# Kernel tuning notes

Hardware: AMD Instinct MI355X
Metric: run time of the kernel (lower is better)

## Reference

```python
import jax, jax.numpy as jnp
import numpy as np

Q_N, S_N, U_N = 5000, 1000, 2000          # questions, skills, users
NQ = NS = NU = NQ2 = 8                     # neighbor fan-outs
D = 100                                    # emb_dim
AGG_HOPS = 3
RANK_K = 10
S_PER_Q = 4                                # skills per question in qs_table
B, T = 32, 100
NEG = -1e30


def linear(x, W, b):
    return x @ W + b


def _forward(fl, it):
    (uq_table, emb_q, emb_q2, emb_s, emb_u, emb_r,
     w1_q, w2_q, w_c, w_p, w_n,
     lstm_Wih, lstm_Whh, lstm_bih, lstm_bhh,
     fusion_W, fusion_b, agg_W, agg_b, agg_last_W, agg_last_b,
     query_W, query_b, key_W, key_b, attn_W, attn_b) = fl
    (user, question, response, mask,
     q_neighbors, s_neighbors, u_neighbors, q_neighbors_2, skill_idx_table) = it

    K_all = emb_q[question]  # [B,T,D] question embeddings for recap scoring

    def build_nodes(root, tabA, tabB):
        # multi-hop neighbor id gather: [B], [B,n0], [B,n0,n1], [B,n0,n1,n2]
        nodes = [root]
        for i in range(AGG_HOPS):
            tab = tabA if i % 2 == 0 else tabB
            nodes.append(tab[nodes[-1]])
        return nodes

    def aggregate(nodes, embA, embB, weighted):
        embs = [(embA if i % 2 == 0 else embB)[n] for i, n in enumerate(nodes)]
        for i in range(AGG_HOPS):
            for j in range(AGG_HOPS - i):
                nb = embs[j + 1]
                if weighted:  # uq branch: edge weights from dense uq_table
                    self_ids, nb_ids = nodes[j], nodes[j + 1]
                    exp_self = jnp.broadcast_to(self_ids[..., None], nb_ids.shape)
                    uid = exp_self if j % 2 == 0 else nb_ids
                    qid = nb_ids if j % 2 == 0 else exp_self
                    w = uq_table[uid, qid]  # [..., 3]
                    fw = w_c * w[..., 0:1] + w_p * w[..., 1:2] + w_n * w[..., 2:3]
                    nb = nb * fw
                s = nb.mean(axis=-2) + embs[j]
                embs[j] = jax.nn.relu(linear(s, agg_W[j], agg_b[j]))
        return jax.nn.relu(linear(embs[0], agg_last_W, agg_last_b))

    def predict(qs_concat, hist, hist_valid):
        # GIKT-style bi-attention readout (source truncated; see notes)
        k = linear(qs_concat, key_W, key_b)    # [B,Nq,D]
        q = linear(hist, query_W, query_b)     # [B,Nh,D]
        Nq, Nh = k.shape[1], q.shape[1]
        feat = jnp.concatenate([
            jnp.broadcast_to(k[:, :, None, :], (B, Nq, Nh, D)),
            jnp.broadcast_to(q[:, None, :, :], (B, Nq, Nh, D))], axis=-1)
        logits = (feat @ attn_W + attn_b)[..., 0]          # [B,Nq,Nh]
        logits = jnp.where(hist_valid[:, None, :], logits, NEG)
        alpha = jax.nn.softmax(logits.reshape(B, -1), axis=1).reshape(B, Nq, Nh)
        inner = jnp.einsum('bqd,bhd->bqh', qs_concat, hist)
        return jax.nn.sigmoid(jnp.sum(alpha * inner, axis=(1, 2)))

    def step(carry, t):
        h, c, state_hist = carry
        m = mask[:, t][:, None]
        u_t, q_t, r_t = user[:, t], question[:, t], response[:, t]
        emb_qt = jnp.where(m, aggregate(build_nodes(q_t, q_neighbors, s_neighbors), emb_q, emb_s, False), emb_q[q_t])
        emb_qt2 = jnp.where(m, aggregate(build_nodes(u_t, u_neighbors, q_neighbors_2), emb_u, emb_q2, True), emb_q2[q_t])
        emb_hat = w1_q * emb_qt + w2_q * emb_qt2
        e_t = jax.nn.relu(linear(jnp.concatenate([emb_hat, emb_r[r_t]], axis=1), fusion_W, fusion_b))
        # LSTMCell (torch gate order i,f,g,o); dropout is identity in eval
        gates = e_t @ lstm_Wih + lstm_bih + h @ lstm_Whh + lstm_bhh
        ig, fg, gg, og = jnp.split(gates, 4, axis=1)
        c_n = jax.nn.sigmoid(fg) * c + jax.nn.sigmoid(ig) * jnp.tanh(gg)
        h_n = jax.nn.sigmoid(og) * jnp.tanh(c_n)
        h = jnp.where(m, h_n, h)
        c = jnp.where(m, c_n, c)
        state_hist = jax.lax.dynamic_update_slice_in_dim(state_hist, h[:, None, :], t, axis=1)
        # recap: question + related skills, current state + top-k history
        q_next = question[:, t + 1]
        emb_qnext = emb_q[q_next]
        qs_concat = jnp.concatenate([emb_qnext[:, None, :], emb_s[skill_idx_table[q_next]]], axis=1)  # [B,1+S_PER_Q,D]
        scores = jnp.einsum('btd,bd->bt', K_all, emb_qnext)
        scores = jnp.where(jnp.arange(T)[None, :] < t, scores, NEG)  # only past steps
        top_s, idx = jax.lax.top_k(scores, RANK_K)
        sel = jnp.take_along_axis(state_hist, idx[:, :, None], axis=1)  # [B,K,D]
        hist = jnp.concatenate([h[:, None, :], sel], axis=1)             # [B,K+1,D]
        hist_valid = jnp.concatenate([jnp.ones((B, 1), bool), top_s > NEG / 2], axis=1)
        return (h, c, state_hist), predict(qs_concat, hist, hist_valid)

    init = (jnp.zeros((B, D), jnp.float32), jnp.zeros((B, D), jnp.float32),
            jnp.zeros((B, T, D), jnp.float32))
    _, ys = jax.lax.scan(jax.checkpoint(step), init, jnp.arange(T - 1))
    return jnp.zeros((B, T), jnp.float32).at[:, 1:].set(ys.T)


def _p(k, shape, scale=0.1):
    return scale * jax.random.normal(k, shape, dtype=jnp.float32)


def setup_inputs():
    key = jax.random.key(0)
    ks = jax.random.split(key, 24)
    rng = np.random.default_rng(0)
    # qs_table with exactly S_PER_Q distinct skills per question -> static skill index table
    qs_idx = np.argsort(rng.random((Q_N, S_N)), axis=1)[:, :S_PER_Q]
    return dict(
        user=jax.random.randint(ks[0], (B, T), 0, U_N),
        question=jax.random.randint(ks[1], (B, T), 0, Q_N),
        response=jax.random.randint(ks[2], (B, T), 0, 2),
        mask=jnp.ones((B, T), dtype=bool),
        q_neighbors=jax.random.randint(ks[3], (Q_N, NQ), 0, S_N),
        s_neighbors=jax.random.randint(ks[4], (S_N, NS), 0, Q_N),
        u_neighbors=jax.random.randint(ks[5], (U_N, NU), 0, Q_N),
        q_neighbors_2=jax.random.randint(ks[6], (Q_N, NQ2), 0, U_N),
        skill_idx_table=jnp.asarray(qs_idx, dtype=jnp.int32),
        uq_table=jax.random.uniform(ks[7], (U_N, Q_N, 3), dtype=jnp.float32),
        emb_q=_p(ks[8], (Q_N, D)), emb_q2=_p(ks[9], (Q_N, D)),
        emb_s=_p(ks[10], (S_N, D)), emb_u=_p(ks[11], (U_N, D)), emb_r=_p(ks[12], (2, D)),
        w1_q=jnp.asarray(0.5, jnp.float32), w2_q=jnp.asarray(0.5, jnp.float32),
        w_c=jnp.asarray(0.33, jnp.float32), w_p=jnp.asarray(0.33, jnp.float32), w_n=jnp.asarray(0.33, jnp.float32),
        lstm_Wih=_p(ks[13], (D, 4 * D)), lstm_Whh=_p(ks[14], (D, 4 * D)),
        lstm_bih=jnp.zeros(4 * D, jnp.float32), lstm_bhh=jnp.zeros(4 * D, jnp.float32),
        fusion_W=_p(ks[15], (2 * D, D)), fusion_b=jnp.zeros(D, jnp.float32),
        agg_W=_p(ks[16], (AGG_HOPS, D, D)), agg_b=jnp.zeros((AGG_HOPS, D), jnp.float32),
        agg_last_W=_p(ks[17], (D, D)), agg_last_b=jnp.zeros(D, jnp.float32),
        query_W=_p(ks[18], (D, D)), query_b=jnp.zeros(D, jnp.float32),
        key_W=_p(ks[19], (D, D)), key_b=jnp.zeros(D, jnp.float32),
        attn_W=_p(ks[20], (2 * D, 1)), attn_b=jnp.zeros(1, jnp.float32),
    )


def reference(user, question, response, mask, q_neighbors, s_neighbors, u_neighbors,
              q_neighbors_2, skill_idx_table, uq_table, emb_q, emb_q2, emb_s, emb_u, emb_r,
              w1_q, w2_q, w_c, w_p, w_n, lstm_Wih, lstm_Whh, lstm_bih, lstm_bhh,
              fusion_W, fusion_b, agg_W, agg_b, agg_last_W, agg_last_b,
              query_W, query_b, key_W, key_b, attn_W, attn_b):
    fl = (uq_table, emb_q, emb_q2, emb_s, emb_u, emb_r,
          w1_q, w2_q, w_c, w_p, w_n,
          lstm_Wih, lstm_Whh, lstm_bih, lstm_bhh,
          fusion_W, fusion_b, agg_W, agg_b, agg_last_W, agg_last_b,
          query_W, query_b, key_W, key_b, attn_W, attn_b)
    it = (user, question, response, mask,
          q_neighbors, s_neighbors, u_neighbors, q_neighbors_2, skill_idx_table)
    return _forward(fl, it)
```

## Files before the change

### kernel.cpp

```cpp
#include <hip/hip_runtime.h>
#include <math.h>

#define Q_N 5000
#define S_N 1000
#define U_N 2000
#define D   100
#define B   32
#define T   100
#define NBT (B*(T-1))
#define NEG_F (-1e30f)

#define NB_Z2Q ((Q_N+15)/16)
#define NB_Z2U ((U_N+15)/16)
#define NB_Y1Q ((S_N+15)/16)
#define NB_Y1U ((Q_N+15)/16)

#define GPROJ_SZ (NBT*4*D)
#define H_SZ     (B*T*D)
#define QAGG_SZ  (Q_N*D)
#define UAGG_SZ  (U_N*D)
#define Z2Q_SZ   (Q_N*D)
#define Z2U_SZ   (U_N*D)
#define Y1Q_SZ   (S_N*D)
#define Y1U_SZ   (Q_N*D)
#define WHT_SZ   (4*D*D)

__device__ __forceinline__ void fma4(float4& a, float s, const float4 w) {
    a.x = fmaf(s, w.x, a.x); a.y = fmaf(s, w.y, a.y);
    a.z = fmaf(s, w.z, a.z); a.w = fmaf(s, w.w, a.w);
}
__device__ __forceinline__ float4 relu4(float4 v) {
    v.x = v.x > 0.f ? v.x : 0.f; v.y = v.y > 0.f ? v.y : 0.f;
    v.z = v.z > 0.f ? v.z : 0.f; v.w = v.w > 0.f ? v.w : 0.f;
    return v;
}
__device__ __forceinline__ float4 add4(float4 a, float4 b) {
    a.x += b.x; a.y += b.y; a.z += b.z; a.w += b.w; return a;
}

template<int K>
__device__ __forceinline__ void mv100_b256(const float* __restrict__ W,
                                           const float* __restrict__ bias,
                                           const float* __restrict__ src,
                                           float* __restrict__ dst,
                                           float* __restrict__ part)
{
    const int tid = threadIdx.x;
    const int c4  = tid & 31;
    const int ks  = tid >> 5;
    const int col0 = (4*c4 < 96) ? 4*c4 : 96;
    float4 acc = {0.f,0.f,0.f,0.f};
#pragma unroll 2
    for (int d = ks*4; d < K; d += 32) {
        const float4 sv = *(const float4*)&src[d];
        const float4 w0 = *(const float4*)&W[(d+0)*D + col0];
        const float4 w1 = *(const float4*)&W[(d+1)*D + col0];
        const float4 w2 = *(const float4*)&W[(d+2)*D + col0];
        const float4 w3 = *(const float4*)&W[(d+3)*D + col0];
        fma4(acc, sv.x, w0); fma4(acc, sv.y, w1);
        fma4(acc, sv.z, w2); fma4(acc, sv.w, w3);
    }
    *(float4*)&part[ks*D + col0] = acc;
    __syncthreads();
    if (tid < D) {
        float v = bias[tid];
#pragma unroll
        for (int k = 0; k < 8; ++k) v += part[k*D + tid];
        dst[tid] = v > 0.f ? v : 0.f;
    }
    __syncthreads();
}

struct __align__(16) Stage16 {
    float x[16*D];
    int   nb[128];
    float fw[128];
};

template<int UQ_MODE>
__device__ __forceinline__ void stage16(Stage16& sh, int row0, int N,
        const float* __restrict__ selfEmb, const float* __restrict__ nbEmb,
        const int* __restrict__ tab,
        const float* __restrict__ uq, float wc, float wp, float wn,
        const float* __restrict__ W, const float* __restrict__ bias,
        float* __restrict__ out)
{
    const int tid = threadIdx.x;
    if (tid < 128) {
        const int i = tid >> 3, k = tid & 7;
        int v = row0 + i; if (v >= N) v = N - 1;
        const int nbv = tab[v*8 + k];
        sh.nb[tid] = nbv;
        float f = 0.125f;
        if (UQ_MODE == 1) {
            const float* w = &uq[(v*Q_N + nbv)*3];
            f = 0.125f*(wc*w[0] + wp*w[1] + wn*w[2]);
        } else if (UQ_MODE == 2) {
            const float* w = &uq[(nbv*Q_N + v)*3];
            f = 0.125f*(wc*w[0] + wp*w[1] + wn*w[2]);
        }
        sh.fw[tid] = f;
    }
    __syncthreads();
    const int c4   = tid & 31;
    const int rowg = tid >> 5;
    const int col0 = (4*c4 < 96) ? 4*c4 : 96;
#pragma unroll
    for (int rr = 0; rr < 2; ++rr) {
        const int i = rowg + 8*rr;
        int v = row0 + i; if (v >= N) v = N - 1;
        float4 acc = *(const float4*)&selfEmb[v*D + col0];
#pragma unroll
        for (int k = 0; k < 8; ++k)
            fma4(acc, sh.fw[i*8 + k], *(const float4*)&nbEmb[sh.nb[i*8 + k]*D + col0]);
        *(float4*)&sh.x[i*D + col0] = acc;
    }
    __syncthreads();
    float4 a0 = {0.f,0.f,0.f,0.f}, a1 = {0.f,0.f,0.f,0.f};
#pragma unroll 1
    for (int d = 0; d < D; d += 4) {
        const float4 w0 = *(const float4*)&W[(d+0)*D + col0];
        const float4 w1 = *(const float4*)&W[(d+1)*D + col0];
        const float4 w2 = *(const float4*)&W[(d+2)*D + col0];
        const float4 w3 = *(const float4*)&W[(d+3)*D + col0];
        const float4 s0 = *(const float4*)&sh.x[rowg*D + d];
        const float4 s1 = *(const float4*)&sh.x[(rowg+8)*D + d];
        fma4(a0, s0.x, w0); fma4(a0, s0.y, w1); fma4(a0, s0.z, w2); fma4(a0, s0.w, w3);
        fma4(a1, s1.x, w0); fma4(a1, s1.y, w1); fma4(a1, s1.z, w2); fma4(a1, s1.w, w3);
    }
    const float4 bb = *(const float4*)&bias[col0];
    {
        int v = row0 + rowg; if (v >= N) v = N - 1;
        *(float4*)&out[v*D + col0] = relu4(add4(a0, bb));
        v = row0 + rowg + 8; if (v >= N) v = N - 1;
        *(float4*)&out[v*D + col0] = relu4(add4(a1, bb));
    }
}

__global__ __launch_bounds__(256, 6)
void kStageA(const int* __restrict__ qnb, const int* __restrict__ snb,
             const int* __restrict__ unb, const int* __restrict__ qnb2,
             const float* __restrict__ emb_q, const float* __restrict__ emb_q2,
             const float* __restrict__ emb_s, const float* __restrict__ emb_u,
             const float* __restrict__ uq,
             const float* __restrict__ wcp, const float* __restrict__ wpp,
             const float* __restrict__ wnp,
             const float* __restrict__ aggW, const float* __restrict__ aggB,
             float* __restrict__ z2q, float* __restrict__ z2u,
             float* __restrict__ y1q0, float* __restrict__ y1u0)
{
    __shared__ Stage16 sh;
    const float wc = wcp[0], wp = wpp[0], wn = wnp[0];
    int b = blockIdx.x;
    if (b < NB_Z2Q) {
        stage16<0>(sh, b*16, Q_N, emb_q, emb_s, qnb, uq, wc, wp, wn,
                   aggW + 2*D*D, aggB + 2*D, z2q);
        return;
    }
    b -= NB_Z2Q;
    if (b < NB_Z2U) {
        stage16<1>(sh, b*16, U_N, emb_u, emb_q2, unb, uq, wc, wp, wn,
                   aggW + 2*D*D, aggB + 2*D, z2u);
        return;
    }
    b -= NB_Z2U;
    if (b < NB_Y1Q) {
        stage16<0>(sh, b*16, S_N, emb_s, emb_q, snb, uq, wc, wp, wn,
                   aggW + 1*D*D, aggB + 1*D, y1q0);
        return;
    }
    b -= NB_Y1Q;
    stage16<2>(sh, b*16, Q_N, emb_q2, emb_u, qnb2, uq, wc, wp, wn,
               aggW + 1*D*D, aggB + 1*D, y1u0);
}

__global__ __launch_bounds__(256, 6)
void kStageB(const int* __restrict__ snb, const int* __restrict__ qnb2,
             const float* __restrict__ uq,
             const float* __restrict__ wcp, const float* __restrict__ wpp,
             const float* __restrict__ wnp,
             const float* __restrict__ aggW, const float* __restrict__ aggB,
             const float* __restrict__ z2q, const float* __restrict__ z2u,
             const float* __restrict__ y1q0, const float* __restrict__ y1u0,
             float* __restrict__ y1q1, float* __restrict__ y1u1)
{
    __shared__ Stage16 sh;
    const float wc = wcp[0], wp = wpp[0], wn = wnp[0];
    int b = blockIdx.x;
    if (b < NB_Y1Q) {
        stage16<0>(sh, b*16, S_N, y1q0, z2q, snb, uq, wc, wp, wn,
                   aggW + 1*D*D, aggB + 1*D, y1q1);
        return;
    }
    b -= NB_Y1Q;
    stage16<2>(sh, b*16, Q_N, y1u0, z2u, qnb2, uq, wc, wp, wn,
               aggW + 1*D*D, aggB + 1*D, y1u1);
}

__global__ void kMarkInit(int* __restrict__ marks)
{
    const int i = blockIdx.x*256 + threadIdx.x;
    if (i < Q_N + U_N) marks[i] = 0;
}
__global__ void kMark(const int* __restrict__ question, const int* __restrict__ user,
                      int* __restrict__ qmark, int* __restrict__ umark)
{
    const int bt = blockIdx.x*256 + threadIdx.x;
    if (bt < NBT) {
        const int b = bt / (T-1), t = bt % (T-1);
        qmark[question[b*T + t]] = 1;
        umark[user[b*T + t]] = 1;
    }
}

__global__ __launch_bounds__(256)
void kTransW(const float* __restrict__ Whh, float* __restrict__ WhhT)
{
    const int i = blockIdx.x*256 + threadIdx.x;
    if (i < 4*D*D) {
        const int c = i / D, d = i - c*D;
        WhhT[i] = Whh[d*4*D + c];
    }
}

struct __align__(16) RootSh {
    float e0[D];
    float part[8*D];
    int   nb[8];
    float fw[8];
};

template<bool WEIGHTED>
__device__ __forceinline__ void rootchain(RootSh& sh, int root,
        const int* __restrict__ tab,
        const float* __restrict__ selfEmb, const float* __restrict__ lvl1Emb,
        const float* __restrict__ y0, const float* __restrict__ y1,
        const float* __restrict__ W0, const float* __restrict__ b0,
        const float* __restrict__ WL, const float* __restrict__ bL,
        const float* __restrict__ uq, float wc, float wp, float wn,
        float* __restrict__ outrow)
{
    const int tid = threadIdx.x;
    if (tid < 8) {
        const int a = tab[root*8 + tid];
        sh.nb[tid] = a;
        float f = 0.125f;
        if (WEIGHTED) {
            const float* w = &uq[(root*Q_N + a)*3];
            f = 0.125f*(wc*w[0] + wp*w[1] + wn*w[2]);
        }
        sh.fw[tid] = f;
    }
    __syncthreads();
    const int c4 = tid & 31;
    const int col0 = (4*c4 < 96) ? 4*c4 : 96;
    if (tid < 32) {
        float4 acc = *(const float4*)&selfEmb[root*D + col0];
#pragma unroll
        for (int k = 0; k < 8; ++k)
            fma4(acc, sh.fw[k], *(const float4*)&lvl1Emb[sh.nb[k]*D + col0]);
        *(float4*)&sh.e0[col0] = acc;
    }
    __syncthreads();
    mv100_b256<D>(W0, b0, sh.e0, sh.e0, sh.part);
    if (tid < 32) {
        float4 acc = *(const float4*)&sh.e0[col0];
#pragma unroll
        for (int k = 0; k < 8; ++k)
            fma4(acc, sh.fw[k], *(const float4*)&y0[sh.nb[k]*D + col0]);
        *(float4*)&sh.e0[col0] = acc;
    }
    __syncthreads();
    mv100_b256<D>(W0, b0, sh.e0, sh.e0, sh.part);
    if (tid < 32) {
        float4 acc = *(const float4*)&sh.e0[col0];
#pragma unroll
        for (int k = 0; k < 8; ++k)
            fma4(acc, sh.fw[k], *(const float4*)&y1[sh.nb[k]*D + col0]);
        *(float4*)&sh.e0[col0] = acc;
    }
    __syncthreads();
    mv100_b256<D>(W0, b0, sh.e0, sh.e0, sh.part);
    mv100_b256<D>(WL, bL, sh.e0, outrow, sh.part);
}

__global__ __launch_bounds__(256, 6)
void kRoot(const int* __restrict__ qmark, const int* __restrict__ umark,
           const int* __restrict__ qnb, const int* __restrict__ unb,
           const float* __restrict__ emb_q, const float* __restrict__ emb_u,
           const float* __restrict__ emb_s, const float* __restrict__ emb_q2,
           const float* __restrict__ y1q0, const float* __restrict__ y1q1,
           const float* __restrict__ y1u0, const float* __restrict__ y1u1,
           const float* __restrict__ uq,
           const float* __restrict__ wcp, const float* __restrict__ wpp,
           const float* __restrict__ wnp,
           const float* __restrict__ aggW, const float* __restrict__ aggB,
           const float* __restrict__ aggLW, const float* __restrict__ aggLb,
           float* __restrict__ qagg, float* __restrict__ uagg)
{
    __shared__ RootSh sh;
    const int b = blockIdx.x;
    if (b < Q_N) {
        if (!qmark[b]) return;
        rootchain<false>(sh, b, qnb, emb_q, emb_s, y1q0, y1q1,
                         aggW, aggB, aggLW, aggLb,
                         uq, 0.f, 0.f, 0.f, qagg + b*D);
    } else {
        const int u = b - Q_N;
        if (!umark[u]) return;
        rootchain<true>(sh, u, unb, emb_u, emb_q2, y1u0, y1u1,
                        aggW, aggB, aggLW, aggLb,
                        uq, wcp[0], wpp[0], wnp[0], uagg + u*D);
    }
}

__global__ __launch_bounds__(256)
void kFuse(const int* __restrict__ question, const int* __restrict__ user,
           const int* __restrict__ response,
           const float* __restrict__ qagg, const float* __restrict__ uagg,
           const float* __restrict__ emb_r,
           const float* __restrict__ w1p, const float* __restrict__ w2p,
           const float* __restrict__ fusW, const float* __restrict__ fusb,
           const float* __restrict__ Wih, const float* __restrict__ bih,
           float* __restrict__ gproj)
{
    __shared__ __align__(16) float xcat[2*D];
    __shared__ __align__(16) float evec[D];
    __shared__ __align__(16) float part[8*D];
    const int bt = blockIdx.x;
    const int b = bt / (T-1);
    const int t = bt % (T-1);
    const int tid = threadIdx.x;
    const int q = question[b*T + t];
    const int u = user[b*T + t];
    const int r = response[b*T + t];
    const float w1 = w1p[0], w2 = w2p[0];
    const int c4 = tid & 31;
    const int col0 = (4*c4 < 96) ? 4*c4 : 96;
    if (tid < 32) {
        float4 qa = *(const float4*)&qagg[q*D + col0];
        float4 ua = *(const float4*)&uagg[u*D + col0];
        float4 x; x.x = w1*qa.x + w2*ua.x; x.y = w1*qa.y + w2*ua.y;
        x.z = w1*qa.z + w2*ua.z; x.w = w1*qa.w + w2*ua.w;
        *(float4*)&xcat[col0] = x;
    } else if (tid < 64) {
        *(float4*)&xcat[D + col0] = *(const float4*)&emb_r[r*D + col0];
    }
    __syncthreads();
    mv100_b256<2*D>(fusW, fusb, xcat, evec, part);

    const int ks = tid >> 7, cw = tid & 127;
    if (cw < D) {
        float4 acc = {0.f,0.f,0.f,0.f};
#pragma unroll 5
        for (int dd = 0; dd < D/2; ++dd) {
            const int d = ks*(D/2) + dd;
            fma4(acc, evec[d], *(const float4*)&Wih[d*4*D + 4*cw]);
        }
        *(float4*)&part[ks*4*D + 4*cw] = acc;
    }
    __syncthreads();
    for (int i = tid; i < 4*D; i += 256) {
        gproj[bt*4*D + i] = part[i] + part[4*D + i] + bih[i];
    }
}

__global__ __launch_bounds__(256)
void kFold(const float* __restrict__ keyW, const float* __restrict__ queryW,
           const float* __restrict__ attnW, float* __restrict__ vk, float* __restrict__ vq)
{
    const int tid = threadIdx.x;
    if (tid < D) {
        float a = 0.f;
        for (int e = 0; e < D; ++e) a = fmaf(keyW[tid*D + e], attnW[e], a);
        vk[tid] = a;
    } else if (tid < 2*D) {
        const int d = tid - D;
        float a = 0.f;
        for (int e = 0; e < D; ++e) a = fmaf(queryW[d*D + e], attnW[D + e], a);
        vq[d] = a;
    }
}

#define KB_LDW(m) const float4 w##m = wvp[m];
#define KB_FMA(m) { const float4 hv = hvp[m]; \
    a0 = fmaf(hv.x, w##m.x, a0); a1 = fmaf(hv.y, w##m.y, a1); \
    a2 = fmaf(hv.z, w##m.z, a2); a3 = fmaf(hv.w, w##m.w, a3); }

__global__ __launch_bounds__(512, 1)
void kB(const float* __restrict__ gproj, const float* __restrict__ WhhT,
        const float* __restrict__ bhh, float* __restrict__ H)
{
    __shared__ __align__(16) float hbuf[D];
    __shared__ float gates[4*D];
    const int b = blockIdx.x;
    const int tid = threadIdx.x;
    const bool on = tid < 4*D;
    const int col = on ? tid : (4*D - 1);
    const float4* wvp = (const float4*)&WhhT[col*D];
    KB_LDW(0)  KB_LDW(1)  KB_LDW(2)  KB_LDW(3)  KB_LDW(4)
    KB_LDW(5)  KB_LDW(6)  KB_LDW(7)  KB_LDW(8)  KB_LDW(9)
    KB_LDW(10) KB_LDW(11) KB_LDW(12) KB_LDW(13) KB_LDW(14)
    KB_LDW(15) KB_LDW(16) KB_LDW(17) KB_LDW(18) KB_LDW(19)
    KB_LDW(20) KB_LDW(21) KB_LDW(22) KB_LDW(23) KB_LDW(24)
    const float bb = bhh[col];
    float creg = 0.f;
    if (tid < D) hbuf[tid] = 0.f;
    float g = on ? gproj[(b*(T-1) + 0)*4*D + col] : 0.f;
    __syncthreads();
#pragma unroll 1
    for (int t = 0; t < T-1; ++t) {
        {
            float a0 = g + bb, a1 = 0.f, a2 = 0.f, a3 = 0.f;
            const float4* hvp = (const float4*)hbuf;
            KB_FMA(0)  KB_FMA(1)  KB_FMA(2)  KB_FMA(3)  KB_FMA(4)
            KB_FMA(5)  KB_FMA(6)  KB_FMA(7)  KB_FMA(8)  KB_FMA(9)
            KB_FMA(10) KB_FMA(11) KB_FMA(12) KB_FMA(13) KB_FMA(14)
            KB_FMA(15) KB_FMA(16) KB_FMA(17) KB_FMA(18) KB_FMA(19)
            KB_FMA(20) KB_FMA(21) KB_FMA(22) KB_FMA(23) KB_FMA(24)
            if (on) gates[tid] = (a0 + a1) + (a2 + a3);
        }
        __syncthreads();
        if (t + 1 < T-1 && on) g = gproj[(b*(T-1) + t + 1)*4*D + col];
        if (tid < D) {
            const float ig = 1.f/(1.f + expf(-gates[tid]));
            const float fg = 1.f/(1.f + expf(-gates[D   + tid]));
            const float gg = tanhf(gates[2*D + tid]);
            const float og = 1.f/(1.f + expf(-gates[3*D + tid]));
            const float cn = fg*creg + ig*gg;
            const float hn = og*tanhf(cn);
            creg = cn;
            hbuf[tid] = hn;
            H[(b*T + t)*D + tid] = hn;
        }
        __syncthreads();
    }
}

__global__ __launch_bounds__(128)
void kC(const int* __restrict__ question, const int* __restrict__ skill_tab,
        const float* __restrict__ emb_q, const float* __restrict__ emb_s,
        const float* __restrict__ H, const float* __restrict__ vk,
        const float* __restrict__ vq, float* __restrict__ out)
{
    __shared__ __align__(16) float qs[5*D];
    __shared__ __align__(16) float hist[11*D];
    __shared__ float scores[T];
    __shared__ float kdot[5], qdot[11];
    __shared__ int   topi[10];
    __shared__ float topv[10];
    const int blk = blockIdx.x;
    const int b = blk / (T-1);
    const int t = blk % (T-1);
    const int tid = threadIdx.x;
    const int qn = question[b*T + t + 1];

    for (int i = tid; i < 5*D; i += 128) {
        const int rr = i / D, d = i % D;
        if (rr == 0) qs[i] = emb_q[qn*D + d];
        else         qs[i] = emb_s[skill_tab[qn*4 + (rr-1)]*D + d];
    }
    __syncthreads();

    for (int tau = tid; tau < T; tau += 128) {
        float sc = NEG_F;
        if (tau < t) {
            const float4* rowp = (const float4*)&emb_q[question[b*T + tau]*D];
            float acc = 0.f;
#pragma unroll 1
            for (int d4 = 0; d4 < D/4; ++d4) {
                const float4 a  = rowp[d4];
                const float4 qv = *(const float4*)&qs[d4*4];
                acc += a.x*qv.x + a.y*qv.y + a.z*qv.z + a.w*qv.w;
            }
            sc = acc;
        }
        scores[tau] = sc;
    }
    __syncthreads();

    for (int k = 0; k < 10; ++k) {
        if (tid < 64) {
            float v = scores[tid]; int idx = tid;
            if (tid + 64 < T) {
                const float v2 = scores[tid + 64];
                if (v2 > v) { v = v2; idx = tid + 64; }
            }
            for (int off = 32; off > 0; off >>= 1) {
                const float ov = __shfl_xor(v, off);
                const int   oi = __shfl_xor(idx, off);
                if (ov > v || (ov == v && oi < idx)) { v = ov; idx = oi; }
            }
            if (tid == 0) { topi[k] = idx; topv[k] = v; scores[idx] = NEG_F; }
        }
        __syncthreads();
    }

    for (int i = tid; i < 11*D; i += 128) {
        const int j = i / D, d = i % D;
        float v;
        if (j == 0) v = H[(b*T + t)*D + d];
        else        v = (topv[j-1] > -5e29f) ? H[(b*T + topi[j-1])*D + d] : 0.f;
        hist[i] = v;
    }
    __syncthreads();

    {
        const int dj = tid >> 3, ks = tid & 7;
        const float* vec = (dj < 5) ? &qs[dj*D] : &hist[(dj-5)*D];
        const float* vv  = (dj < 5) ? vk : vq;
        float a = 0.f;
#pragma unroll
        for (int d = ks; d < D; d += 8) a = fmaf(vec[d], vv[d], a);
        a += __shfl_xor(a, 1); a += __shfl_xor(a, 2); a += __shfl_xor(a, 4);
        if (ks == 0) { if (dj < 5) kdot[dj] = a; else qdot[dj-5] = a; }
    }
    __syncthreads();

    if (tid < 64) {
        const int i = tid / 11, j = tid - i*11;
        const bool act = tid < 55;
        const bool valid = act && (j == 0 || topv[j-1] > -5e29f);
        float logit = valid ? (kdot[i] + qdot[j]) : NEG_F;
        float mx = logit;
        for (int off = 32; off > 0; off >>= 1) mx = fmaxf(mx, __shfl_xor(mx, off));
        const float e = valid ? expf(logit - mx) : 0.f;
        float inner = 0.f;
        if (act) {
#pragma unroll
            for (int d4 = 0; d4 < D/4; ++d4) {
                const float4 a4 = *(const float4*)&qs[i*D + d4*4];
                const float4 h4 = *(const float4*)&hist[j*D + d4*4];
                inner += a4.x*h4.x + a4.y*h4.y + a4.z*h4.z + a4.w*h4.w;
            }
        }
        float num = e * inner;
        float den = e;
        for (int off = 32; off > 0; off >>= 1) {
            num += __shfl_xor(num, off);
            den += __shfl_xor(den, off);
        }
        if (tid == 0) {
            out[b*T + t + 1] = 1.f/(1.f + expf(-(num/den)));
            if (t == 0) out[b*T] = 0.f;
        }
    }
}

extern "C" void kernel_launch(void* const* d_in, const int* in_sizes, int n_in,
                              void* d_out, int out_size, void* d_ws, size_t ws_size,
                              hipStream_t stream)
{
    const int*   user     = (const int*)d_in[0];
    const int*   question = (const int*)d_in[1];
    const int*   response = (const int*)d_in[2];
    const int*   qnb   = (const int*)d_in[4];
    const int*   snb   = (const int*)d_in[5];
    const int*   unb   = (const int*)d_in[6];
    const int*   qnb2  = (const int*)d_in[7];
    const int*   skill = (const int*)d_in[8];
    const float* uq    = (const float*)d_in[9];
    const float* emb_q  = (const float*)d_in[10];
    const float* emb_q2 = (const float*)d_in[11];
    const float* emb_s  = (const float*)d_in[12];
    const float* emb_u  = (const float*)d_in[13];
    const float* emb_r  = (const float*)d_in[14];
    const float* w1 = (const float*)d_in[15];
    const float* w2 = (const float*)d_in[16];
    const float* wc = (const float*)d_in[17];
    const float* wp = (const float*)d_in[18];
    const float* wn = (const float*)d_in[19];
    const float* Wih = (const float*)d_in[20];
    const float* Whh = (const float*)d_in[21];
    const float* bih = (const float*)d_in[22];
    const float* bhh = (const float*)d_in[23];
    const float* fusW = (const float*)d_in[24];
    const float* fusb = (const float*)d_in[25];
    const float* aggW = (const float*)d_in[26];
    const float* aggB = (const float*)d_in[27];
    const float* aggLW = (const float*)d_in[28];
    const float* aggLb = (const float*)d_in[29];
    const float* queryW = (const float*)d_in[30];
    const float* keyW   = (const float*)d_in[32];
    const float* attnW  = (const float*)d_in[34];

    float* ws    = (float*)d_ws;
    float* gproj = ws;
    float* H     = gproj + GPROJ_SZ;
    float* vk    = H + H_SZ;
    float* vq    = vk + D;
    float* qagg  = vq + D;
    float* uagg  = qagg + QAGG_SZ;
    float* z2q   = uagg + UAGG_SZ;
    float* z2u   = z2q + Z2Q_SZ;
    float* y1q0  = z2u + Z2U_SZ;
    float* y1q1  = y1q0 + Y1Q_SZ;
    float* y1u0  = y1q1 + Y1Q_SZ;
    float* y1u1  = y1u0 + Y1U_SZ;
    float* whhT  = y1u1 + Y1U_SZ;
    int*   qmark = (int*)(whhT + WHT_SZ);
    int*   umark = qmark + Q_N;
    float* out   = (float*)d_out;

    const size_t need = (size_t)(GPROJ_SZ + H_SZ + 2*D + QAGG_SZ + UAGG_SZ
                       + Z2Q_SZ + Z2U_SZ + 2*Y1Q_SZ + 2*Y1U_SZ + WHT_SZ)*sizeof(float)
                       + (size_t)(Q_N + U_N)*sizeof(int);
    if (ws_size < need) return;

    kMarkInit<<<dim3((Q_N + U_N + 255)/256), dim3(256), 0, stream>>>(qmark);
    kMark<<<dim3((NBT + 255)/256), dim3(256), 0, stream>>>(question, user, qmark, umark);
    kTransW<<<dim3((4*D*D + 255)/256), dim3(256), 0, stream>>>(Whh, whhT);
    kStageA<<<dim3(NB_Z2Q + NB_Z2U + NB_Y1Q + NB_Y1U), dim3(256), 0, stream>>>(
        qnb, snb, unb, qnb2, emb_q, emb_q2, emb_s, emb_u, uq, wc, wp, wn,
        aggW, aggB, z2q, z2u, y1q0, y1u0);
    kStageB<<<dim3(NB_Y1Q + NB_Y1U), dim3(256), 0, stream>>>(
        snb, qnb2, uq, wc, wp, wn, aggW, aggB, z2q, z2u, y1q0, y1u0, y1q1, y1u1);
    kRoot<<<dim3(Q_N + U_N), dim3(256), 0, stream>>>(
        qmark, umark, qnb, unb, emb_q, emb_u, emb_s, emb_q2,
        y1q0, y1q1, y1u0, y1u1, uq, wc, wp, wn,
        aggW, aggB, aggLW, aggLb, qagg, uagg);
    kFold<<<dim3(1), dim3(256), 0, stream>>>(keyW, queryW, attnW, vk, vq);
    kFuse<<<dim3(NBT), dim3(256), 0, stream>>>(question, user, response, qagg, uagg,
        emb_r, w1, w2, fusW, fusb, Wih, bih, gproj);
    kB<<<dim3(B), dim3(512), 0, stream>>>(gproj, whhT, bhh, H);
    kC<<<dim3(NBT), dim3(128), 0, stream>>>(question, skill, emb_q, emb_s, H, vk, vq, out);
}
```

Baseline: 279.9 us.

## Fuse setup kernels and broadcast LSTM hidden state via readlane in recurrence

Merges the mark, weight-transpose and attention-fold kernels into one setup launch, cutting launch count. In the serial LSTM kernel, each wave loads the hidden vector once from shared memory as float2 per lane and broadcasts elements with readlane instead of issuing many LDS float4 reads per thread. Gate activations are moved into the 400-thread matvec phase so the 100-thread update phase only does the cell math. The readlane path adds scalar-register traffic and changes the occupancy attributes.

```diff
diff --git a/kernel.cpp b/kernel.cpp
--- a/kernel.cpp
+++ b/kernel.cpp
@@ -14,6 +14,8 @@
 #define NB_Z2U ((U_N+15)/16)
 #define NB_Y1Q ((S_N+15)/16)
 #define NB_Y1U ((Q_N+15)/16)
+#define NB_MK ((NBT+255)/256)
+#define NB_TW ((4*D*D+255)/256)
 
 #define GPROJ_SZ (NBT*4*D)
 #define H_SZ     (B*T*D)
@@ -202,24 +204,44 @@
     const int i = blockIdx.x*256 + threadIdx.x;
     if (i < Q_N + U_N) marks[i] = 0;
 }
-__global__ void kMark(const int* __restrict__ question, const int* __restrict__ user,
-                      int* __restrict__ qmark, int* __restrict__ umark)
-{
-    const int bt = blockIdx.x*256 + threadIdx.x;
-    if (bt < NBT) {
-        const int b = bt / (T-1), t = bt % (T-1);
-        qmark[question[b*T + t]] = 1;
-        umark[user[b*T + t]] = 1;
-    }
-}
 
 __global__ __launch_bounds__(256)
-void kTransW(const float* __restrict__ Whh, float* __restrict__ WhhT)
-{
-    const int i = blockIdx.x*256 + threadIdx.x;
-    if (i < 4*D*D) {
-        const int c = i / D, d = i - c*D;
-        WhhT[i] = Whh[d*4*D + c];
+void kSetup(const int* __restrict__ question, const int* __restrict__ user,
+            int* __restrict__ qmark, int* __restrict__ umark,
+            const float* __restrict__ Whh, float* __restrict__ WhhT,
+            const float* __restrict__ keyW, const float* __restrict__ queryW,
+            const float* __restrict__ attnW,
+            float* __restrict__ vk, float* __restrict__ vq)
+{
+    int bkt = blockIdx.x;
+    const int tid = threadIdx.x;
+    if (bkt < NB_MK) {
+        const int bt = bkt*256 + tid;
+        if (bt < NBT) {
+            const int b = bt / (T-1), t = bt % (T-1);
+            qmark[question[b*T + t]] = 1;
+            umark[user[b*T + t]] = 1;
+        }
+        return;
+    }
+    bkt -= NB_MK;
+    if (bkt < NB_TW) {
+        const int i = bkt*256 + tid;
+        if (i < 4*D*D) {
+            const int c = i / D, d = i - c*D;
+            WhhT[i] = Whh[d*4*D + c];
+        }
+        return;
+    }
+    if (tid < D) {
+        float a = 0.f;
+        for (int e = 0; e < D; ++e) a = fmaf(keyW[tid*D + e], attnW[e], a);
+        vk[tid] = a;
+    } else if (tid < 2*D) {
+        const int d = tid - D;
+        float a = 0.f;
+        for (int e = 0; e < D; ++e) a = fmaf(queryW[d*D + e], attnW[D + e], a);
+        vq[d] = a;
     }
 }
 
@@ -365,68 +387,61 @@
     }
 }
 
-__global__ __launch_bounds__(256)
-void kFold(const float* __restrict__ keyW, const float* __restrict__ queryW,
-           const float* __restrict__ attnW, float* __restrict__ vk, float* __restrict__ vq)
-{
-    const int tid = threadIdx.x;
-    if (tid < D) {
-        float a = 0.f;
-        for (int e = 0; e < D; ++e) a = fmaf(keyW[tid*D + e], attnW[e], a);
-        vk[tid] = a;
-    } else if (tid < 2*D) {
-        const int d = tid - D;
-        float a = 0.f;
-        for (int e = 0; e < D; ++e) a = fmaf(queryW[d*D + e], attnW[D + e], a);
-        vq[d] = a;
-    }
-}
-
-#define KB_LDW(m) const float4 w##m = wvp[m];
-#define KB_FMA(m) { const float4 hv = hvp[m]; \
-    a0 = fmaf(hv.x, w##m.x, a0); a1 = fmaf(hv.y, w##m.y, a1); \
-    a2 = fmaf(hv.z, w##m.z, a2); a3 = fmaf(hv.w, w##m.w, a3); }
-
-__global__ __launch_bounds__(512, 1)
+#define KBW_LD(m) const float4 W##m = wvp[m];
+#define HVAL(d) __int_as_float(__builtin_amdgcn_readlane(((d) & 1) ? h1i : h0i, (d) >> 1))
+#define KBW_FMA(m) \
+    a0 = fmaf(HVAL(4*(m)+0), W##m.x, a0); \
+    a1 = fmaf(HVAL(4*(m)+1), W##m.y, a1); \
+    a2 = fmaf(HVAL(4*(m)+2), W##m.z, a2); \
+    a3 = fmaf(HVAL(4*(m)+3), W##m.w, a3);
+
+__global__ __attribute__((amdgpu_flat_work_group_size(512, 512)))
+           __attribute__((amdgpu_waves_per_eu(2, 2)))
 void kB(const float* __restrict__ gproj, const float* __restrict__ WhhT,
         const float* __restrict__ bhh, float* __restrict__ H)
 {
-    __shared__ __align__(16) float hbuf[D];
+    __shared__ __align__(16) float hbuf[104];
     __shared__ float gates[4*D];
     const int b = blockIdx.x;
     const int tid = threadIdx.x;
     const bool on = tid < 4*D;
     const int col = on ? tid : (4*D - 1);
+    const float bb = bhh[col];
+    const bool isG = (col >= 2*D) && (col < 3*D);
     const float4* wvp = (const float4*)&WhhT[col*D];
-    KB_LDW(0)  KB_LDW(1)  KB_LDW(2)  KB_LDW(3)  KB_LDW(4)
-    KB_LDW(5)  KB_LDW(6)  KB_LDW(7)  KB_LDW(8)  KB_LDW(9)
-    KB_LDW(10) KB_LDW(11) KB_LDW(12) KB_LDW(13) KB_LDW(14)
-    KB_LDW(15) KB_LDW(16) KB_LDW(17) KB_LDW(18) KB_LDW(19)
-    KB_LDW(20) KB_LDW(21) KB_LDW(22) KB_LDW(23) KB_LDW(24)
-    const float bb = bhh[col];
+    KBW_LD(0)  KBW_LD(1)  KBW_LD(2)  KBW_LD(3)  KBW_LD(4)
+    KBW_LD(5)  KBW_LD(6)  KBW_LD(7)  KBW_LD(8)  KBW_LD(9)
+    KBW_LD(10) KBW_LD(11) KBW_LD(12) KBW_LD(13) KBW_LD(14)
+    KBW_LD(15) KBW_LD(16) KBW_LD(17) KBW_LD(18) KBW_LD(19)
+    KBW_LD(20) KBW_LD(21) KBW_LD(22) KBW_LD(23) KBW_LD(24)
+    const int lane = tid & 63;
+    const int ll = (lane < 52) ? lane : 51;
     float creg = 0.f;
-    if (tid < D) hbuf[tid] = 0.f;
+    if (tid < 104) hbuf[tid] = 0.f;
     float g = on ? gproj[(b*(T-1) + 0)*4*D + col] : 0.f;
     __syncthreads();
 #pragma unroll 1
     for (int t = 0; t < T-1; ++t) {
-        {
+        const float2 hh = *(const float2*)&hbuf[2*ll];
+        const int h0i = __float_as_int(hh.x);
+        const int h1i = __float_as_int(hh.y);
+        if (on) {
             float a0 = g + bb, a1 = 0.f, a2 = 0.f, a3 = 0.f;
-            const float4* hvp = (const float4*)hbuf;
-            KB_FMA(0)  KB_FMA(1)  KB_FMA(2)  KB_FMA(3)  KB_FMA(4)
-            KB_FMA(5)  KB_FMA(6)  KB_FMA(7)  KB_FMA(8)  KB_FMA(9)
-            KB_FMA(10) KB_FMA(11) KB_FMA(12) KB_FMA(13) KB_FMA(14)
-            KB_FMA(15) KB_FMA(16) KB_FMA(17) KB_FMA(18) KB_FMA(19)
-            KB_FMA(20) KB_FMA(21) KB_FMA(22) KB_FMA(23) KB_FMA(24)
-            if (on) gates[tid] = (a0 + a1) + (a2 + a3);
+            KBW_FMA(0)  KBW_FMA(1)  KBW_FMA(2)  KBW_FMA(3)  KBW_FMA(4)
+            KBW_FMA(5)  KBW_FMA(6)  KBW_FMA(7)  KBW_FMA(8)  KBW_FMA(9)
+            KBW_FMA(10) KBW_FMA(11) KBW_FMA(12) KBW_FMA(13) KBW_FMA(14)
+            KBW_FMA(15) KBW_FMA(16) KBW_FMA(17) KBW_FMA(18) KBW_FMA(19)
+            KBW_FMA(20) KBW_FMA(21) KBW_FMA(22) KBW_FMA(23) KBW_FMA(24)
+            const float tot = (a0 + a1) + (a2 + a3);
+            gates[col] = isG ? tanhf(tot) : 1.f/(1.f + expf(-tot));
         }
         __syncthreads();
         if (t + 1 < T-1 && on) g = gproj[(b*(T-1) + t + 1)*4*D + col];
         if (tid < D) {
-            const float ig = 1.f/(1.f + expf(-gates[tid]));
-            const float fg = 1.f/(1.f + expf(-gates[D   + tid]));
-            const float gg = tanhf(gates[2*D + tid]);
-            const float og = 1.f/(1.f + expf(-gates[3*D + tid]));
+            const float ig = gates[tid];
+            const float fg = gates[D   + tid];
+            const float gg = gates[2*D + tid];
+            const float og = gates[3*D + tid];
             const float cn = fg*creg + ig*gg;
             const float hn = og*tanhf(cn);
             creg = cn;
@@ -608,8 +623,8 @@
     if (ws_size < need) return;
 
     kMarkInit<<<dim3((Q_N + U_N + 255)/256), dim3(256), 0, stream>>>(qmark);
-    kMark<<<dim3((NBT + 255)/256), dim3(256), 0, stream>>>(question, user, qmark, umark);
-    kTransW<<<dim3((4*D*D + 255)/256), dim3(256), 0, stream>>>(Whh, whhT);
+    kSetup<<<dim3(NB_MK + NB_TW + 1), dim3(256), 0, stream>>>(
+        question, user, qmark, umark, Whh, whhT, keyW, queryW, attnW, vk, vq);
     kStageA<<<dim3(NB_Z2Q + NB_Z2U + NB_Y1Q + NB_Y1U), dim3(256), 0, stream>>>(
         qnb, snb, unb, qnb2, emb_q, emb_q2, emb_s, emb_u, uq, wc, wp, wn,
         aggW, aggB, z2q, z2u, y1q0, y1u0);
@@ -619,7 +634,6 @@
         qmark, umark, qnb, unb, emb_q, emb_u, emb_s, emb_q2,
         y1q0, y1q1, y1u0, y1u1, uq, wc, wp, wn,
         aggW, aggB, aggLW, aggLb, qagg, uagg);
-    kFold<<<dim3(1), dim3(256), 0, stream>>>(keyW, queryW, attnW, vk, vq);
     kFuse<<<dim3(NBT), dim3(256), 0, stream>>>(question, user, response, qagg, uagg,
         emb_r, w1, w2, fusW, fusb, Wih, bih, gproj);
     kB<<<dim3(B), dim3(512), 0, stream>>>(gproj, whhT, bhh, H);
```

New measurement: 266.2 us. -4.9%, faster.
